# Optimization experiments

Hardware: AMD Instinct MI355X
Metric: run time of the kernel (lower is better)

## Reference

```python
import jax, jax.numpy as jnp
jax.config.update("jax_enable_x64", True)
import numpy as np

# Dimensions from init_kwargs
B = 1024            # batch of binarized input patterns
T = 4096            # total_input_bits
N = 4096            # num_neurons
NB = 16             # n_bits_per_neuron
MEM_SIZE = 1 << NB  # 65536 addressable cells per neuron
BITS_PER_CELL = 2
CELLS_PER_WORD = 62 // BITS_PER_CELL          # 31
WPN = (MEM_SIZE + CELLS_PER_WORD - 1) // CELLS_PER_WORD  # 2115 words per neuron


def setup_inputs() -> dict:
    key = jax.random.key(0)
    k1, k2, k3 = jax.random.split(key, 3)
    # binarized input patterns in {0,1}
    x = jax.random.randint(k1, (B, T), 0, 2, dtype=jnp.int32)
    # per-neuron connections into the input bit vector
    connections = jax.random.randint(k2, (N, NB), 0, T, dtype=jnp.int64)
    # bit-packed 2-bit RAM cells (trained state); random words stand in for a
    # trained memory -- the read math is identical regardless of contents
    memory_words = jax.random.randint(k3, (N, WPN), 0, 2**31 - 1, dtype=jnp.int64)
    return {"x": x, "connections": connections, "memory_words": memory_words}


def reference(x, connections, memory_words):
    # Gather each neuron's connected input bits: [B, N, NB]
    bits = jnp.take(x, connections, axis=1).astype(jnp.int64)
    # MSB-first address decode (matches binary_addresses = 2**arange(NB-1,-1,-1))
    weights = (jnp.int64(1) << jnp.arange(NB - 1, -1, -1, dtype=jnp.int64))
    addr = jnp.sum(bits * weights, axis=-1)  # [B, N] in [0, MEM_SIZE)
    # _cell_coords: locate the packed 2-bit cell
    word_index = addr // CELLS_PER_WORD          # [B, N]
    bit_shift = (addr % CELLS_PER_WORD) * BITS_PER_CELL
    # Irregular gather of the packed words: memory_words[n, word_index[b, n]]
    words = memory_words[jnp.arange(N, dtype=jnp.int64)[None, :], word_index]  # [B, N]
    # _read_cells: extract 2-bit cell value in {0,1,2} (FALSE, TRUE, EMPTY)
    vals = (words >> bit_shift) & 3
    return vals
```

## Files before the change

kernel.cpp:

```cpp
#include <hip/hip_runtime.h>
#include <stdint.h>

constexpr int Tdim = 4096;
constexpr int Ndim = 4096;
constexpr int Bdim = 1024;
constexpr int NB   = 16;
constexpr int WPN  = 2115;

__device__ __forceinline__ int probe_stride(const int* __restrict__ p) {
    const int l = threadIdx.x & 63;
    return (__ballot(p[2 * l + 1] == 0) == ~0ull) ? 2 : 1;
}

__global__ __launch_bounds__(256) void pack_kernel(const int* __restrict__ x,
                                                   uint32_t* __restrict__ xT) {
    const int sx = probe_stride(x);
    const int t  = blockIdx.x * 256 + threadIdx.x;
    const int bg = blockIdx.y;
    uint32_t w = 0;
#pragma unroll
    for (int bl = 0; bl < 32; ++bl) {
        const size_t idx = ((size_t)(bg * 32 + bl) * Tdim + t) * sx;
        w |= (uint32_t)(x[idx] & 1) << bl;
    }
    xT[(size_t)bg * Tdim + t] = w;
}

__global__ __launch_bounds__(512) void row_kernel(const uint32_t* __restrict__ xT,
                                                  const int* __restrict__ conn,
                                                  const int* __restrict__ mem,
                                                  int* __restrict__ out) {
    const int sc = probe_stride(conn);
    const int sm = probe_stride(mem);

    const int l = threadIdx.x & 63;
    const int w = threadIdx.x >> 6;
    const int n = blockIdx.x * 8 + w;

    __shared__ int tile[64 * 9];

    int c[16];
    const int* cp = conn + (size_t)n * NB * sc;
#pragma unroll
    for (int j = 0; j < 16; ++j) c[j] = cp[j * sc];

    const int* mrow = mem + (size_t)n * WPN * sm;
    const int bit = l & 31;

    for (int g = 0; g < 16; ++g) {
        const uint32_t* xs = xT + (size_t)(g * 2 + (l >> 5)) * Tdim;
        uint32_t addr = 0;
#pragma unroll
        for (int j = 0; j < 16; ++j)
            addr = (addr << 1) | ((xs[c[j]] >> bit) & 1u);

        const uint32_t wi = addr / 31u;
        const uint32_t sh = (addr - wi * 31u) * 2u;
        const uint64_t wd = (uint32_t)mrow[(size_t)wi * sm];
        tile[l * 9 + w] = (int)((wd >> sh) & 3u);
        __syncthreads();
        const int r  = threadIdx.x >> 3;
        const int c2 = threadIdx.x & 7;
        out[(size_t)(g * 64 + r) * Ndim + blockIdx.x * 8 + c2] = tile[r * 9 + c2];
        __syncthreads();
    }
}

__global__ __launch_bounds__(256) void direct_kernel(const int* __restrict__ x,
                                                     const int* __restrict__ conn,
                                                     const int* __restrict__ mem,
                                                     int* __restrict__ out) {
    const int sx = probe_stride(x);
    const int sc = probe_stride(conn);
    const int sm = probe_stride(mem);
    const int n  = blockIdx.x * 256 + threadIdx.x;
    const int b  = blockIdx.y;
    const int* cp = conn + (size_t)n * NB * sc;
    const int* xr = x + (size_t)b * Tdim * sx;
    uint32_t addr = 0;
#pragma unroll
    for (int j = 0; j < 16; ++j)
        addr = (addr << 1) | (uint32_t)(xr[(size_t)cp[j * sc] * sx] & 1);
    const uint32_t wi = addr / 31u;
    const uint32_t sh = (addr - wi * 31u) * 2u;
    const uint64_t wd = (uint32_t)mem[((size_t)n * WPN + wi) * sm];
    out[(size_t)b * Ndim + n] = (int)((wd >> sh) & 3u);
}

extern "C" void kernel_launch(void* const* d_in, const int* in_sizes, int n_in,
                              void* d_out, int out_size, void* d_ws, size_t ws_size,
                              hipStream_t stream) {
    const int* x    = (const int*)d_in[0];
    const int* conn = (const int*)d_in[1];
    const int* mem  = (const int*)d_in[2];
    int*       out  = (int*)d_out;
    uint32_t*  xT   = (uint32_t*)d_ws;

    const size_t need = (size_t)(Bdim / 32) * Tdim * sizeof(uint32_t);
    if (ws_size >= need) {
        dim3 g1(Tdim / 256, Bdim / 32);
        pack_kernel<<<g1, 256, 0, stream>>>(x, xT);
        row_kernel<<<Ndim / 8, 512, 0, stream>>>(xT, conn, mem, out);
    } else {
        dim3 g3(Ndim / 256, Bdim);
        direct_kernel<<<g3, 256, 0, stream>>>(x, conn, mem, out);
    }
}
```

Before: 122.3 us.

## Stage gathered input bits in LDS and transpose outputs via ballot masks

Each row_kernel block now covers 16 neurons and half the batch, using 1024 threads on a 2D grid. The 16 connected packed-bit words per batch group are gathered once into shared memory, so the 16x16 scattered global xT reads are not repeated per thread. Output values are turned into 64-bit ballot masks stored in LDS, and a single transposed store pass replaces the per-iteration tile write and two __syncthreads. In exchange it uses more LDS per block and a larger block size, which may lower occupancy. The grid also changes from 512 to 512 blocks of doubled size, split across two batch halves.

```diff
diff --git a/kernel.cpp b/kernel.cpp
--- a/kernel.cpp
+++ b/kernel.cpp
@@ -26,43 +26,65 @@
     xT[(size_t)bg * Tdim + t] = w;
 }
 
-__global__ __launch_bounds__(512) void row_kernel(const uint32_t* __restrict__ xT,
-                                                  const int* __restrict__ conn,
-                                                  const int* __restrict__ mem,
-                                                  int* __restrict__ out) {
+__global__ __launch_bounds__(1024) void row_kernel(const uint32_t* __restrict__ xT,
+                                                   const int* __restrict__ conn,
+                                                   const int* __restrict__ mem,
+                                                   int* __restrict__ out) {
     const int sc = probe_stride(conn);
     const int sm = probe_stride(mem);
 
-    const int l = threadIdx.x & 63;
-    const int w = threadIdx.x >> 6;
-    const int n = blockIdx.x * 8 + w;
+    const int tid = threadIdx.x;
+    const int l   = tid & 63;
+    const int w   = tid >> 6;
+    const int n   = blockIdx.x * 16 + w;
+    const int by  = blockIdx.y;
 
-    __shared__ int tile[64 * 9];
+    __shared__ uint32_t bits[16 * 256];
+    __shared__ uint64_t msk[2][16][9];
 
-    int c[16];
-    const int* cp = conn + (size_t)n * NB * sc;
+    const int jhi  = l >> 4;
+    const int bgl  = l & 15;
+    const int cbase = n * NB * sc;
 #pragma unroll
-    for (int j = 0; j < 16; ++j) c[j] = cp[j * sc];
+    for (int k = 0; k < 4; ++k) {
+        const int j = k * 4 + jhi;
+        const int c = conn[cbase + j * sc];
+        bits[w * 256 + j * 16 + bgl] =
+            xT[(size_t)(by * 16 + bgl) * Tdim + c];
+    }
 
     const int* mrow = mem + (size_t)n * WPN * sm;
+    const uint32_t* myb = &bits[w * 256];
+    const int hib = l >> 5;
     const int bit = l & 31;
 
-    for (int g = 0; g < 16; ++g) {
-        const uint32_t* xs = xT + (size_t)(g * 2 + (l >> 5)) * Tdim;
+#pragma unroll
+    for (int p = 0; p < 8; ++p) {
+        const int bg = p * 2 + hib;
         uint32_t addr = 0;
 #pragma unroll
         for (int j = 0; j < 16; ++j)
-            addr = (addr << 1) | ((xs[c[j]] >> bit) & 1u);
+            addr = (addr << 1) | ((myb[j * 16 + bg] >> bit) & 1u);
 
         const uint32_t wi = addr / 31u;
         const uint32_t sh = (addr - wi * 31u) * 2u;
         const uint64_t wd = (uint32_t)mrow[(size_t)wi * sm];
-        tile[l * 9 + w] = (int)((wd >> sh) & 3u);
-        __syncthreads();
-        const int r  = threadIdx.x >> 3;
-        const int c2 = threadIdx.x & 7;
-        out[(size_t)(g * 64 + r) * Ndim + blockIdx.x * 8 + c2] = tile[r * 9 + c2];
-        __syncthreads();
+        const uint32_t v  = (uint32_t)((wd >> sh) & 3u);
+        const uint64_t b0 = __ballot((v & 1u) != 0u);
+        const uint64_t b1 = __ballot((v & 2u) != 0u);
+        if (l == 0) { msk[0][w][p] = b0; msk[1][w][p] = b1; }
+    }
+    __syncthreads();
+
+    const int nl = tid & 15;
+    const int s  = tid >> 4;
+#pragma unroll
+    for (int q = 0; q < 8; ++q) {
+        const uint64_t m0 = msk[0][nl][q];
+        const uint64_t m1 = msk[1][nl][q];
+        const int v = (int)((m0 >> s) & 1ull) | ((int)((m1 >> s) & 1ull) << 1);
+        const int b = by * 512 + q * 64 + s;
+        out[(size_t)b * Ndim + blockIdx.x * 16 + nl] = v;
     }
 }
 
@@ -100,7 +122,8 @@
     if (ws_size >= need) {
         dim3 g1(Tdim / 256, Bdim / 32);
         pack_kernel<<<g1, 256, 0, stream>>>(x, xT);
-        row_kernel<<<Ndim / 8, 512, 0, stream>>>(xT, conn, mem, out);
+        dim3 g2(Ndim / 16, Bdim / 512);
+        row_kernel<<<g2, 1024, 0, stream>>>(xT, conn, mem, out);
     } else {
         dim3 g3(Ndim / 256, Bdim);
         direct_kernel<<<g3, 256, 0, stream>>>(x, conn, mem, out);
```

After: 115.9 us. -5.2%, faster.

## Stage neuron memory rows and gathered bits in LDS, pack outputs via ballots

Applied to the files above, without the earlier changes.

Each block now handles two neurons. It loads both full packed memory rows (2×2115 words) and all gathered input-bit words into shared memory, then does the address decode and the cell lookup from LDS instead of scattered global reads. Cell values are compressed into wave ballot masks and written out as coalesced pairs per batch row. A blockIdx swizzle is added. The cost is about 17KB of LDS per block and output stores that only cover two adjacent neurons per row, which gives short 8-byte segments.

```diff
diff --git a/kernel.cpp b/kernel.cpp
--- a/kernel.cpp
+++ b/kernel.cpp
@@ -26,43 +26,90 @@
     xT[(size_t)bg * Tdim + t] = w;
 }
 
-__global__ __launch_bounds__(512) void row_kernel(const uint32_t* __restrict__ xT,
+__global__ __launch_bounds__(256) void row_kernel(const uint32_t* __restrict__ xT,
                                                   const int* __restrict__ conn,
                                                   const int* __restrict__ mem,
                                                   int* __restrict__ out) {
     const int sc = probe_stride(conn);
     const int sm = probe_stride(mem);
 
-    const int l = threadIdx.x & 63;
-    const int w = threadIdx.x >> 6;
-    const int n = blockIdx.x * 8 + w;
+    const int i  = blockIdx.x;
+    const int bx = (i & 255) * 8 + (i >> 8);
+    const int n0 = bx * 2;
 
-    __shared__ int tile[64 * 9];
+    const int tid = threadIdx.x;
 
-    int c[16];
-    const int* cp = conn + (size_t)n * NB * sc;
+    __shared__ uint32_t rowbuf[2 * WPN];
+    __shared__ uint32_t bits[2 * 32 * 16];
+    __shared__ uint64_t omask[2][16][2];
+
+    const size_t base = (size_t)n0 * WPN;
+    if (sm == 2) {
+        const uint2* m2 = (const uint2*)mem;
 #pragma unroll
-    for (int j = 0; j < 16; ++j) c[j] = cp[j * sc];
+        for (int k = 0; k < 17; ++k) {
+            const int idx = k * 256 + tid;
+            if (idx < 2 * WPN) rowbuf[idx] = m2[base + idx].x;
+        }
+    } else {
+        const uint32_t* m1 = (const uint32_t*)mem;
+#pragma unroll
+        for (int k = 0; k < 17; ++k) {
+            const int idx = k * 256 + tid;
+            if (idx < 2 * WPN) rowbuf[idx] = m1[base + idx];
+        }
+    }
 
-    const int* mrow = mem + (size_t)n * WPN * sm;
+#pragma unroll
+    for (int k = 0; k < 4; ++k) {
+        const int idx = k * 256 + tid;
+        const int n_l = idx >> 9;
+        const int bg  = (idx >> 4) & 31;
+        const int j   = idx & 15;
+        const int c   = conn[((n0 + n_l) * NB + j) * sc];
+        bits[idx] = xT[(size_t)bg * Tdim + c];
+    }
+    __syncthreads();
+
+    const int w   = tid >> 6;
+    const int l   = tid & 63;
     const int bit = l & 31;
+    const int hi  = l >> 5;
+#pragma unroll
+    for (int n_l = 0; n_l < 2; ++n_l) {
+        const uint32_t* myrow = &rowbuf[n_l * WPN];
+        const uint32_t* myb   = &bits[n_l * 512];
+#pragma unroll
+        for (int it = 0; it < 4; ++it) {
+            const int bg = w * 8 + it * 2 + hi;
+            const uint32_t* bp = &myb[bg * 16];
+            uint32_t addr = 0;
+#pragma unroll
+            for (int j = 0; j < 16; ++j)
+                addr = (addr << 1) | ((bp[j] >> bit) & 1u);
+            const uint32_t wi = addr / 31u;
+            const uint32_t sh = (addr - wi * 31u) * 2u;
+            const uint32_t v = (uint32_t)(((uint64_t)myrow[wi] >> sh) & 3ull);
+            const uint64_t b0 = __ballot((v & 1u) != 0u);
+            const uint64_t b1 = __ballot((v & 2u) != 0u);
+            if (l == 0) {
+                omask[n_l][w * 4 + it][0] = b0;
+                omask[n_l][w * 4 + it][1] = b1;
+            }
+        }
+    }
+    __syncthreads();
 
-    for (int g = 0; g < 16; ++g) {
-        const uint32_t* xs = xT + (size_t)(g * 2 + (l >> 5)) * Tdim;
-        uint32_t addr = 0;
 #pragma unroll
-        for (int j = 0; j < 16; ++j)
-            addr = (addr << 1) | ((xs[c[j]] >> bit) & 1u);
-
-        const uint32_t wi = addr / 31u;
-        const uint32_t sh = (addr - wi * 31u) * 2u;
-        const uint64_t wd = (uint32_t)mrow[(size_t)wi * sm];
-        tile[l * 9 + w] = (int)((wd >> sh) & 3u);
-        __syncthreads();
-        const int r  = threadIdx.x >> 3;
-        const int c2 = threadIdx.x & 7;
-        out[(size_t)(g * 64 + r) * Ndim + blockIdx.x * 8 + c2] = tile[r * 9 + c2];
-        __syncthreads();
+    for (int k = 0; k < 8; ++k) {
+        const int t2  = k * 256 + tid;
+        const int n_l = t2 & 1;
+        const int b   = t2 >> 1;
+        const uint64_t m0 = omask[n_l][b >> 6][0];
+        const uint64_t m1 = omask[n_l][b >> 6][1];
+        const int s = b & 63;
+        const int v = (int)((m0 >> s) & 1ull) | ((int)((m1 >> s) & 1ull) << 1);
+        out[(size_t)b * Ndim + n0 + n_l] = v;
     }
 }
 
@@ -100,7 +147,7 @@
     if (ws_size >= need) {
         dim3 g1(Tdim / 256, Bdim / 32);
         pack_kernel<<<g1, 256, 0, stream>>>(x, xT);
-        row_kernel<<<Ndim / 8, 512, 0, stream>>>(xT, conn, mem, out);
+        row_kernel<<<Ndim / 2, 256, 0, stream>>>(xT, conn, mem, out);
     } else {
         dim3 g3(Ndim / 256, Bdim);
         direct_kernel<<<g3, 256, 0, stream>>>(x, conn, mem, out);
```

Measured after the change: 125.3 us. 1.02x slower.
